# Performance work log

Hardware: AMD Instinct MI355X
Metric: run time of the kernel (lower is better)

The kernel has to match this reference:

```python
import jax, jax.numpy as jnp
import numpy as np

N = 100000   # nodes
E = 1600000  # edges (before self-loops)
F_IN = 128
H = 64
G = 512      # graphs in batch


def _add_self_loops(edge_index, n):
    loop = jnp.arange(n, dtype=edge_index.dtype)
    src = jnp.concatenate([edge_index[0], loop])
    dst = jnp.concatenate([edge_index[1], loop])
    return src, dst


def _gcn_norm(src, dst, n):
    # PyG GCNConv: deg over targets with self-loops, norm = d^-1/2[src]*d^-1/2[dst]
    deg = jax.ops.segment_sum(jnp.ones_like(dst, dtype=jnp.float32), dst, num_segments=n)
    dinv = jnp.where(deg > 0, jax.lax.rsqrt(deg), 0.0)
    return dinv[src] * dinv[dst]


def _gcn_conv(x, src, dst, norm, W, b):
    xw = x @ W                                # [N, H]
    msg = xw[src] * norm[:, None]             # [E+N, H] gather + scale
    out = jax.ops.segment_sum(msg, dst, num_segments=x.shape[0])
    return out + b


def setup_inputs() -> dict:
    key = jax.random.key(0)
    ks = jax.random.split(key, 9)
    x = jax.random.normal(ks[0], (N, F_IN), dtype=jnp.float32)
    edge_index = jax.random.randint(ks[1], (2, E), 0, N, dtype=jnp.int32)
    batch = jnp.sort(jax.random.randint(ks[2], (N,), 0, G, dtype=jnp.int32))
    s1 = 1.0 / np.sqrt(F_IN)
    s2 = 1.0 / np.sqrt(H)
    W1 = jax.random.uniform(ks[3], (F_IN, H), jnp.float32, -s1, s1)
    b1 = jnp.zeros((H,), jnp.float32)
    W2 = jax.random.uniform(ks[4], (H, H), jnp.float32, -s2, s2)
    b2 = jnp.zeros((H,), jnp.float32)
    Wl = jax.random.uniform(ks[5], (H, 1), jnp.float32, -s2, s2)
    bl = jnp.zeros((1,), jnp.float32)
    return {"x": x, "edge_index": edge_index, "batch": batch,
            "W1": W1, "b1": b1, "W2": W2, "b2": b2, "Wl": Wl, "bl": bl}


def reference(x, edge_index, batch, W1, b1, W2, b2, Wl, bl):
    n = x.shape[0]
    src, dst = _add_self_loops(edge_index, n)
    norm = _gcn_norm(src, dst, n)
    h = jax.nn.relu(_gcn_conv(x, src, dst, norm, W1, b1))
    h = jax.nn.relu(_gcn_conv(h, src, dst, norm, W2, b2))
    # global mean pool over graphs
    sums = jax.ops.segment_sum(h, batch, num_segments=G)          # [G, H]
    cnt = jax.ops.segment_sum(jnp.ones((n,), jnp.float32), batch, num_segments=G)
    pooled = sums / jnp.maximum(cnt, 1.0)[:, None]
    return jax.nn.sigmoid(pooled @ Wl + bl)                        # [G, 1]
```

## Files before the change

kernel.cpp:

```cpp
#include <hip/hip_runtime.h>
#include <hip/hip_bf16.h>
#include <cmath>

#define F_IN 128
#define HDIM 64
#define NPB 128
#define NB1 512
#define CAP 2560

typedef __attribute__((ext_vector_type(8))) short bf16x8;
typedef __attribute__((ext_vector_type(4))) float f32x4;
typedef __attribute__((ext_vector_type(2))) float f32x2;

__device__ __forceinline__ float bf2f(unsigned short u) {
    union { unsigned int i; float f; } v; v.i = ((unsigned int)u) << 16; return v.f;
}
__device__ __forceinline__ unsigned short f2bf(float f) {
    __hip_bfloat16 h = __float2bfloat16(f);
    union { __hip_bfloat16 h; unsigned short u; } c; c.h = h; return c.u;
}
__device__ __forceinline__ unsigned char f2fp8(float f) {
    int p = __builtin_amdgcn_cvt_pk_fp8_f32(f, f, 0, false);
    return (unsigned char)(p & 0xff);
}
__device__ __forceinline__ void fp8x8_acc(uint2 v, float* a) {
    f32x2 f;
    f = __builtin_amdgcn_cvt_pk_f32_fp8(v.x, false); a[0] += f.x; a[1] += f.y;
    f = __builtin_amdgcn_cvt_pk_f32_fp8(v.x, true);  a[2] += f.x; a[3] += f.y;
    f = __builtin_amdgcn_cvt_pk_f32_fp8(v.y, false); a[4] += f.x; a[5] += f.y;
    f = __builtin_amdgcn_cvt_pk_f32_fp8(v.y, true);  a[6] += f.x; a[7] += f.y;
}


__launch_bounds__(256)
__global__ void p0_count(const int* __restrict__ dst, int* __restrict__ blk_cnt,
                         int E, int nbuk, int chunk,
                         const float* __restrict__ W1, const float* __restrict__ W2,
                         unsigned short* __restrict__ w1t, unsigned short* __restrict__ w2t) {
    int tid = threadIdx.x;
    if (blockIdx.x >= NB1) {
        int t = (blockIdx.x - NB1) * 256 + tid;
        if (t < F_IN * 64) {
            int c = t & 63, k = t >> 6;
            w1t[c * F_IN + k] = f2bf(W1[t]);
        } else if (t < F_IN * 64 + HDIM * 64) {
            int u = t - F_IN * 64;
            int c = u & 63, k = u >> 6;
            w2t[c * HDIM + k] = f2bf(W2[u]);
        }
        return;
    }
    __shared__ int hist[1024];
    for (int i = tid; i < nbuk; i += 256) hist[i] = 0;
    __syncthreads();
    int lo = blockIdx.x * chunk, hi = min(E, lo + chunk);
    for (int e = lo + tid; e < hi; e += 256)
        atomicAdd(&hist[dst[e] >> 7], 1);
    __syncthreads();
    for (int i = tid; i < nbuk; i += 256)
        blk_cnt[(size_t)i * NB1 + blockIdx.x] = hist[i];
}


__launch_bounds__(256)
__global__ void p_scan_blocks(int* __restrict__ blk_cnt, int* __restrict__ bucket_cnt,
                              int nbuk, const int* __restrict__ batch,
                              int* __restrict__ gstart, int n, int G) {
    int tid = threadIdx.x;
    if (blockIdx.x >= nbuk) {
        int g = (blockIdx.x - nbuk) * 256 + tid;
        if (g > G) return;
        int lo = 0, hi = n;
        while (lo < hi) {
            int mid = (lo + hi) >> 1;
            if (batch[mid] < g) lo = mid + 1; else hi = mid;
        }
        gstart[g] = lo;
        return;
    }
    __shared__ int sd[256];
    int b = blockIdx.x;
    int2* row = (int2*)(blk_cnt + (size_t)b * NB1);
    int2 v = row[tid];
    int s0 = v.x, s1 = s0 + v.y;
    sd[tid] = s1;
    __syncthreads();
    for (int off = 1; off < 256; off <<= 1) {
        int a = (tid >= off) ? sd[tid - off] : 0;
        __syncthreads();
        sd[tid] += a;
        __syncthreads();
    }
    int base = sd[tid] - s1;
    row[tid] = make_int2(base, base + s0);
    if (tid == 255) bucket_cnt[b] = sd[255];
}


__launch_bounds__(256)
__global__ void p1_place(const int* __restrict__ src, const int* __restrict__ dst,
                         const int* __restrict__ blk_cnt, int* __restrict__ pairs,
                         int E, int nbuk, int chunk) {
    __shared__ int cur[1024];
    int tid = threadIdx.x;
    for (int i = tid; i < nbuk; i += 256)
        cur[i] = i * CAP + blk_cnt[(size_t)i * NB1 + blockIdx.x];
    __syncthreads();
    int lo = blockIdx.x * chunk, hi = min(E, lo + chunk);
    for (int e = lo + tid; e < hi; e += 256) {
        int d = dst[e];
        int pos = atomicAdd(&cur[d >> 7], 1);
        pairs[pos] = (src[e] << 7) | (d & 127);
    }
}


__launch_bounds__(256)
__global__ void p2_csr(const int* __restrict__ pairs, const int* __restrict__ bucket_cnt,
                       float* __restrict__ dinv, int* __restrict__ col,
                       int4* __restrict__ slot_hdr, int n) {
    __shared__ int dl[128];
    __shared__ int sc[128];
    __shared__ int cur[128];
    __shared__ int h64[64];
    __shared__ int s64[64];
    int b = blockIdx.x, tid = threadIdx.x;
    int nlo = b << 7;
    int eb = b * CAP;
    int ee = eb + bucket_cnt[b];
    if (tid < 128) dl[tid] = 0;
    if (tid < 64) h64[tid] = 0;
    __syncthreads();
    for (int e = eb + tid; e < ee; e += 256)
        atomicAdd(&dl[pairs[e] & 127], 1);
    __syncthreads();
    int d0 = 0, excl = 0;
    if (tid < 128) { d0 = dl[tid]; sc[tid] = d0; }
    __syncthreads();
    for (int off = 1; off < 128; off <<= 1) {
        int a = (tid >= off && tid < 128) ? sc[tid - off] : 0;
        __syncthreads();
        if (tid < 128) sc[tid] += a;
        __syncthreads();
    }
    if (tid < 128) {
        excl = sc[tid] - d0;
        int node = nlo + tid;
        float dv = rsqrtf((float)(d0 + 1));
        if (node < n) dinv[node] = dv;
        cur[tid] = eb + excl;
        atomicAdd(&h64[min(d0, 63)], 1);
    }
    __syncthreads();
    if (tid == 0) { int run = 0; for (int i = 0; i < 64; ++i) { s64[i] = run; run += h64[i]; } }
    __syncthreads();
    if (tid < 64) h64[tid] = 0;
    __syncthreads();
    if (tid < 128) {
        int node = nlo + tid;
        int bin = min(d0, 63);
        int pos = s64[bin] + atomicAdd(&h64[bin], 1);
        int4 hdr;
        hdr.x = (node < n) ? node : 0x7fffffff;
        hdr.y = eb + excl;
        hdr.z = d0;
        hdr.w = __float_as_int(rsqrtf((float)(d0 + 1)));
        slot_hdr[nlo + pos] = hdr;
    }
    __syncthreads();
    for (int e = eb + tid; e < ee; e += 256) {
        unsigned int v = (unsigned int)pairs[e];
        int pos = atomicAdd(&cur[v & 127], 1);
        col[pos] = (int)(v >> 7);
    }
}


template <int K>
__launch_bounds__(256)
__global__ void matmul_mfma(const float* __restrict__ X, const unsigned short* __restrict__ Wt,
                            const float* __restrict__ dinv, unsigned char* __restrict__ out,
                            int n) {
    constexpr int KS  = K / 32;
    constexpr int LDX = K + 8;
    __shared__ unsigned short Xs[64 * LDX];
    __shared__ unsigned short Ws[64 * LDX];
    int tid = threadIdx.x;
    int rowbase = blockIdx.x * 64;
    for (int i = tid; i < 64 * (K / 8); i += 256) {
        int r = i / (K / 8), ch = i % (K / 8);
        *(bf16x8*)(Ws + r * LDX + ch * 8) = ((const bf16x8*)Wt)[i];
    }
    {
        const float4* X4 = (const float4*)X;
        for (int i = tid; i < 64 * (K / 4); i += 256) {
            int r = i / (K / 4), k4 = i % (K / 4);
            ushort4 u = { 0, 0, 0, 0 };
            int gr = rowbase + r;
            if (gr < n) {
                float4 v = X4[(size_t)gr * (K / 4) + k4];
                u.x = f2bf(v.x); u.y = f2bf(v.y); u.z = f2bf(v.z); u.w = f2bf(v.w);
            }
            *(ushort4*)(Xs + r * LDX + k4 * 4) = u;
        }
    }
    __syncthreads();
    int wave = tid >> 6, lane = tid & 63;
    int q = lane >> 4, nn = lane & 15;
    f32x4 acc[4] = {{0,0,0,0},{0,0,0,0},{0,0,0,0},{0,0,0,0}};
    int mrow = wave * 16 + nn;
#pragma unroll
    for (int s = 0; s < KS; ++s) {
        bf16x8 af = *(const bf16x8*)(Xs + mrow * LDX + s * 32 + q * 8);
#pragma unroll
        for (int c = 0; c < 4; ++c) {
            bf16x8 bf = *(const bf16x8*)(Ws + (c * 16 + nn) * LDX + s * 32 + q * 8);
            acc[c] = __builtin_amdgcn_mfma_f32_16x16x32_bf16(af, bf, acc[c], 0, 0, 0);
        }
    }
#pragma unroll
    for (int r = 0; r < 4; ++r) {
        int row = rowbase + wave * 16 + q * 4 + r;
        if (row >= n) continue;
        float dv = dinv[row];
#pragma unroll
        for (int c = 0; c < 4; ++c)
            out[(size_t)row * HDIM + c * 16 + nn] = f2fp8(acc[c][r] * dv);
    }
}


__launch_bounds__(256)
__global__ void gather1_mm2(const int4* __restrict__ slot_hdr, const int* __restrict__ col,
                            const uint2* __restrict__ xws, const float* __restrict__ bias,
                            const unsigned short* __restrict__ w2t,
                            unsigned char* __restrict__ out8, int nslots, int n) {
    __shared__ unsigned short Hs[32 * 72];
    __shared__ unsigned short Ws[64 * 72];
    __shared__ int   snode[32];
    __shared__ float sdinv[32];

    int tid = threadIdx.x;
    int ls = tid >> 3;
    int L  = tid & 7;
    int slot = blockIdx.x * 32 + ls;

    for (int i = tid; i < 64 * 8; i += 256) {
        int r = i >> 3, ch = i & 7;
        *(bf16x8*)(Ws + r * 72 + ch * 8) = ((const bf16x8*)w2t)[i];
    }

    int node = 0x7fffffff;
    float dv = 0.0f;
    float a[8] = {0, 0, 0, 0, 0, 0, 0, 0};
    if (slot < nslots) {
        int4 hdr = slot_hdr[slot];
        node = hdr.x;
        if (node < n) {
            int s = hdr.y, end = s + hdr.z;
            dv = __int_as_float(hdr.w);
            fp8x8_acc(xws[(size_t)node * 8 + L], a);
            int e = s;
            for (; e + 8 <= end; e += 8) {
                uint2 v0 = xws[(size_t)col[e + 0] * 8 + L];
                uint2 v1 = xws[(size_t)col[e + 1] * 8 + L];
                uint2 v2 = xws[(size_t)col[e + 2] * 8 + L];
                uint2 v3 = xws[(size_t)col[e + 3] * 8 + L];
                uint2 v4 = xws[(size_t)col[e + 4] * 8 + L];
                uint2 v5 = xws[(size_t)col[e + 5] * 8 + L];
                uint2 v6 = xws[(size_t)col[e + 6] * 8 + L];
                uint2 v7 = xws[(size_t)col[e + 7] * 8 + L];
                fp8x8_acc(v0, a); fp8x8_acc(v1, a); fp8x8_acc(v2, a); fp8x8_acc(v3, a);
                fp8x8_acc(v4, a); fp8x8_acc(v5, a); fp8x8_acc(v6, a); fp8x8_acc(v7, a);
            }
            for (; e < end; ++e)
                fp8x8_acc(xws[(size_t)col[e] * 8 + L], a);
        }
    }
    if (L == 0) { snode[ls] = node; sdinv[ls] = dv; }
    {
        int f0 = L * 8;
        bf16x8 o;
        if (node < n) {
#pragma unroll
            for (int j = 0; j < 8; ++j)
                o[j] = (short)f2bf(fmaxf(fmaf(a[j], dv, bias[f0 + j]), 0.0f));
        } else {
            short z[8] = {0,0,0,0,0,0,0,0};
            o = *(bf16x8*)z;
        }
        *(bf16x8*)(Hs + ls * 72 + L * 8) = o;
    }
    __syncthreads();

    int wave = tid >> 6, lane = tid & 63;
    int q = lane >> 4, nn = lane & 15;
    int mt  = wave & 1;
    int nt0 = (wave >> 1) * 2;
    f32x4 acc[2] = {{0,0,0,0},{0,0,0,0}};
#pragma unroll
    for (int s = 0; s < 2; ++s) {
        bf16x8 af = *(const bf16x8*)(Hs + (mt * 16 + nn) * 72 + s * 32 + q * 8);
#pragma unroll
        for (int t = 0; t < 2; ++t) {
            bf16x8 bf = *(const bf16x8*)(Ws + ((nt0 + t) * 16 + nn) * 72 + s * 32 + q * 8);
            acc[t] = __builtin_amdgcn_mfma_f32_16x16x32_bf16(af, bf, acc[t], 0, 0, 0);
        }
    }
#pragma unroll
    for (int r = 0; r < 4; ++r) {
        int lslot = mt * 16 + q * 4 + r;
        int nd = snode[lslot];
        if (nd >= n) continue;
        float dvr = sdinv[lslot];
#pragma unroll
        for (int t = 0; t < 2; ++t)
            out8[(size_t)nd * HDIM + (nt0 + t) * 16 + nn] = f2fp8(acc[t][r] * dvr);
    }
}


__launch_bounds__(256)
__global__ void csr_gather8_fp8(const int4* __restrict__ slot_hdr, const int* __restrict__ col,
                                const uint2* __restrict__ xws, const float* __restrict__ bias,
                                bf16x8* __restrict__ outb, int nslots, int n) {
    int t = blockIdx.x * 256 + threadIdx.x;
    int slot = t >> 3;
    if (slot >= nslots) return;
    int L = t & 7;
    int4 hdr = slot_hdr[slot];
    int node = hdr.x;
    if (node >= n) return;
    int s = hdr.y, end = s + hdr.z;
    float dv = __int_as_float(hdr.w);

    float a[8] = {0, 0, 0, 0, 0, 0, 0, 0};
    fp8x8_acc(xws[(size_t)node * 8 + L], a);
    int e = s;
    for (; e + 8 <= end; e += 8) {
        uint2 v0 = xws[(size_t)col[e + 0] * 8 + L];
        uint2 v1 = xws[(size_t)col[e + 1] * 8 + L];
        uint2 v2 = xws[(size_t)col[e + 2] * 8 + L];
        uint2 v3 = xws[(size_t)col[e + 3] * 8 + L];
        uint2 v4 = xws[(size_t)col[e + 4] * 8 + L];
        uint2 v5 = xws[(size_t)col[e + 5] * 8 + L];
        uint2 v6 = xws[(size_t)col[e + 6] * 8 + L];
        uint2 v7 = xws[(size_t)col[e + 7] * 8 + L];
        fp8x8_acc(v0, a); fp8x8_acc(v1, a); fp8x8_acc(v2, a); fp8x8_acc(v3, a);
        fp8x8_acc(v4, a); fp8x8_acc(v5, a); fp8x8_acc(v6, a); fp8x8_acc(v7, a);
    }
    for (; e < end; ++e)
        fp8x8_acc(xws[(size_t)col[e] * 8 + L], a);

    int f0 = L * 8;
    bf16x8 o;
#pragma unroll
    for (int j = 0; j < 8; ++j)
        o[j] = (short)f2bf(fmaxf(fmaf(a[j], dv, bias[f0 + j]), 0.0f));
    outb[(size_t)node * 8 + L] = o;
}


__launch_bounds__(256)
__global__ void pool_head(const unsigned short* __restrict__ h, const int* __restrict__ gstart,
                          const float* __restrict__ Wl, const float* __restrict__ bl,
                          float* __restrict__ out, int G) {
    int g = blockIdx.x;
    int s = gstart[g], e = gstart[g + 1];
    int f  = threadIdx.x & 63;
    int rg = threadIdx.x >> 6;
    float acc = 0.0f;
    for (int i = s + rg; i < e; i += 4)
        acc += bf2f(h[(size_t)i * HDIM + f]);
    __shared__ float red[4][HDIM];
    red[rg][f] = acc;
    __syncthreads();
    if (rg == 0) {
        float v = (red[0][f] + red[1][f]) + (red[2][f] + red[3][f]);
        float c = fmaxf((float)(e - s), 1.0f);
        v = v * Wl[f] * (1.0f / c);
#pragma unroll
        for (int off = 32; off; off >>= 1) v += __shfl_down(v, off, 64);
        if (f == 0) out[g] = 1.0f / (1.0f + expf(-(v + bl[0])));
    }
}


extern "C" void kernel_launch(void* const* d_in, const int* in_sizes, int n_in,
                              void* d_out, int out_size, void* d_ws, size_t ws_size,
                              hipStream_t stream) {
    const float* x   = (const float*)d_in[0];
    const int* ei    = (const int*)d_in[1];
    const int* batch = (const int*)d_in[2];
    const float* W1  = (const float*)d_in[3];
    const float* b1  = (const float*)d_in[4];
    const float* W2  = (const float*)d_in[5];
    const float* b2  = (const float*)d_in[6];
    const float* Wl  = (const float*)d_in[7];
    const float* bl  = (const float*)d_in[8];
    float* out = (float*)d_out;

    const int n = in_sizes[0] / F_IN;
    const int E = in_sizes[1] / 2;
    const int G = out_size;

    const int* srcp = ei;
    const int* dstp = ei + E;

    int nbuk = (n + NPB - 1) / NPB;
    int nslots = nbuk * NPB;

    char* wsb = (char*)d_ws;
    auto alloc = [&](size_t bytes) { char* p = wsb; wsb += (bytes + 255) & ~(size_t)255; return p; };
    float* dinv       = (float*)alloc((size_t)n * 4);
    int4*  slot_hdr   = (int4*)alloc((size_t)nslots * 16);
    int*   bucket_cnt = (int*)alloc(1024 * 4);
    int*   blk_cnt    = (int*)alloc((size_t)nbuk * NB1 * 4);
    int*   pairs      = (int*)alloc((size_t)nbuk * CAP * 4);
    int*   colx       = (int*)alloc((size_t)nbuk * CAP * 4);
    unsigned short* w1t  = (unsigned short*)alloc((size_t)F_IN * HDIM * 2);
    unsigned short* w2t  = (unsigned short*)alloc((size_t)HDIM * HDIM * 2);
    unsigned char*  xws8 = (unsigned char*)alloc((size_t)n * HDIM);
    unsigned char*  xws8b= (unsigned char*)alloc((size_t)n * HDIM);
    unsigned short* xh2  = (unsigned short*)alloc((size_t)n * HDIM * 2);
    int*   gstart     = (int*)alloc(((size_t)G + 1) * 4);

    const int TB = 256;
    int gMM  = (n + 63) / 64;
    int chunk = (E + NB1 - 1) / NB1;
    int gG8  = (nslots * 8 + TB - 1) / TB;
    int gS   = (nslots + 31) / 32;

    p0_count<<<NB1 + 48, TB, 0, stream>>>(dstp, blk_cnt, E, nbuk, chunk, W1, W2, w1t, w2t);
    p_scan_blocks<<<nbuk + 3, TB, 0, stream>>>(blk_cnt, bucket_cnt, nbuk, batch, gstart, n, G);
    p1_place<<<NB1, TB, 0, stream>>>(srcp, dstp, blk_cnt, pairs, E, nbuk, chunk);
    p2_csr<<<nbuk, TB, 0, stream>>>(pairs, bucket_cnt, dinv, colx, slot_hdr, n);

    matmul_mfma<F_IN><<<gMM, TB, 0, stream>>>(x, w1t, dinv, xws8, n);
    gather1_mm2<<<gS, TB, 0, stream>>>(slot_hdr, colx, (const uint2*)xws8,
                                       b1, w2t, xws8b, nslots, n);
    csr_gather8_fp8<<<gG8, TB, 0, stream>>>(slot_hdr, colx, (const uint2*)xws8b,
                                            b2, (bf16x8*)xh2, nslots, n);
    pool_head<<<G, TB, 0, stream>>>(xh2, gstart, Wl, bl, out, G);
}
```

Measured before the change: 238.8 us.

## Replace count/scan bucketing with atomic bucket offsets and stage pairs in LDS

Merges the per-block histogram, cross-block scan and placement kernels into one placement kernel. Each block now claims its range within each bucket by doing a global atomicAdd on a per-bucket counter, so two launches and the blk_cnt matrix traffic go away. The CSR build caches the bucket's pairs in shared memory so they are read from global memory only once, and the tail of the neighbor gather becomes one masked 8-wide batch instead of a scalar loop. The cost is nondeterministic edge order within a bucket, which changes the float summation order, plus added LDS use in p2_csr that may lower occupancy.

```diff
diff --git a/kernel.cpp b/kernel.cpp
--- a/kernel.cpp
+++ b/kernel.cpp
@@ -30,46 +30,72 @@
     f = __builtin_amdgcn_cvt_pk_f32_fp8(v.y, false); a[4] += f.x; a[5] += f.y;
     f = __builtin_amdgcn_cvt_pk_f32_fp8(v.y, true);  a[6] += f.x; a[7] += f.y;
 }
-
-
-__launch_bounds__(256)
-__global__ void p0_count(const int* __restrict__ dst, int* __restrict__ blk_cnt,
-                         int E, int nbuk, int chunk,
-                         const float* __restrict__ W1, const float* __restrict__ W2,
-                         unsigned short* __restrict__ w1t, unsigned short* __restrict__ w2t) {
-    int tid = threadIdx.x;
-    if (blockIdx.x >= NB1) {
-        int t = (blockIdx.x - NB1) * 256 + tid;
-        if (t < F_IN * 64) {
-            int c = t & 63, k = t >> 6;
-            w1t[c * F_IN + k] = f2bf(W1[t]);
-        } else if (t < F_IN * 64 + HDIM * 64) {
-            int u = t - F_IN * 64;
-            int c = u & 63, k = u >> 6;
-            w2t[c * HDIM + k] = f2bf(W2[u]);
-        }
+__device__ __forceinline__ void fp8x8_acc_m(uint2 v, float m, float* a) {
+    f32x2 f;
+    f = __builtin_amdgcn_cvt_pk_f32_fp8(v.x, false); a[0] = fmaf(f.x, m, a[0]); a[1] = fmaf(f.y, m, a[1]);
+    f = __builtin_amdgcn_cvt_pk_f32_fp8(v.x, true);  a[2] = fmaf(f.x, m, a[2]); a[3] = fmaf(f.y, m, a[3]);
+    f = __builtin_amdgcn_cvt_pk_f32_fp8(v.y, false); a[4] = fmaf(f.x, m, a[4]); a[5] = fmaf(f.y, m, a[5]);
+    f = __builtin_amdgcn_cvt_pk_f32_fp8(v.y, true);  a[6] = fmaf(f.x, m, a[6]); a[7] = fmaf(f.y, m, a[7]);
+}
+
+__device__ __forceinline__ void gather_rows(const int* __restrict__ col,
+                                            const uint2* __restrict__ xws,
+                                            int L, int s, int end, float* a) {
+    int e = s;
+    for (; e + 8 <= end; e += 8) {
+        uint2 v0 = xws[(size_t)col[e + 0] * 8 + L];
+        uint2 v1 = xws[(size_t)col[e + 1] * 8 + L];
+        uint2 v2 = xws[(size_t)col[e + 2] * 8 + L];
+        uint2 v3 = xws[(size_t)col[e + 3] * 8 + L];
+        uint2 v4 = xws[(size_t)col[e + 4] * 8 + L];
+        uint2 v5 = xws[(size_t)col[e + 5] * 8 + L];
+        uint2 v6 = xws[(size_t)col[e + 6] * 8 + L];
+        uint2 v7 = xws[(size_t)col[e + 7] * 8 + L];
+        fp8x8_acc(v0, a); fp8x8_acc(v1, a); fp8x8_acc(v2, a); fp8x8_acc(v3, a);
+        fp8x8_acc(v4, a); fp8x8_acc(v5, a); fp8x8_acc(v6, a); fp8x8_acc(v7, a);
+    }
+    if (e < end) {
+        int last = end - 1;
+        uint2 v0 = xws[(size_t)col[e]               * 8 + L];
+        uint2 v1 = xws[(size_t)col[min(e + 1, last)] * 8 + L];
+        uint2 v2 = xws[(size_t)col[min(e + 2, last)] * 8 + L];
+        uint2 v3 = xws[(size_t)col[min(e + 3, last)] * 8 + L];
+        uint2 v4 = xws[(size_t)col[min(e + 4, last)] * 8 + L];
+        uint2 v5 = xws[(size_t)col[min(e + 5, last)] * 8 + L];
+        uint2 v6 = xws[(size_t)col[min(e + 6, last)] * 8 + L];
+        uint2 v7 = xws[(size_t)col[min(e + 7, last)] * 8 + L];
+        fp8x8_acc(v0, a);
+        fp8x8_acc_m(v1, (e + 1 < end) ? 1.0f : 0.0f, a);
+        fp8x8_acc_m(v2, (e + 2 < end) ? 1.0f : 0.0f, a);
+        fp8x8_acc_m(v3, (e + 3 < end) ? 1.0f : 0.0f, a);
+        fp8x8_acc_m(v4, (e + 4 < end) ? 1.0f : 0.0f, a);
+        fp8x8_acc_m(v5, (e + 5 < end) ? 1.0f : 0.0f, a);
+        fp8x8_acc_m(v6, (e + 6 < end) ? 1.0f : 0.0f, a);
+        fp8x8_acc_m(v7, (e + 7 < end) ? 1.0f : 0.0f, a);
+    }
+}
+
+
+__launch_bounds__(256)
+__global__ void k_init(const float* __restrict__ W1, const float* __restrict__ W2,
+                       unsigned short* __restrict__ w1t, unsigned short* __restrict__ w2t,
+                       const int* __restrict__ batch, int* __restrict__ gstart,
+                       int n, int G, int* __restrict__ gcnt) {
+    int t = blockIdx.x * 256 + threadIdx.x;
+    if (t < F_IN * 64) {
+        int c = t & 63, k = t >> 6;
+        w1t[c * F_IN + k] = f2bf(W1[t]);
         return;
     }
-    __shared__ int hist[1024];
-    for (int i = tid; i < nbuk; i += 256) hist[i] = 0;
-    __syncthreads();
-    int lo = blockIdx.x * chunk, hi = min(E, lo + chunk);
-    for (int e = lo + tid; e < hi; e += 256)
-        atomicAdd(&hist[dst[e] >> 7], 1);
-    __syncthreads();
-    for (int i = tid; i < nbuk; i += 256)
-        blk_cnt[(size_t)i * NB1 + blockIdx.x] = hist[i];
-}
-
-
-__launch_bounds__(256)
-__global__ void p_scan_blocks(int* __restrict__ blk_cnt, int* __restrict__ bucket_cnt,
-                              int nbuk, const int* __restrict__ batch,
-                              int* __restrict__ gstart, int n, int G) {
-    int tid = threadIdx.x;
-    if (blockIdx.x >= nbuk) {
-        int g = (blockIdx.x - nbuk) * 256 + tid;
-        if (g > G) return;
+    t -= F_IN * 64;
+    if (t < HDIM * 64) {
+        int c = t & 63, k = t >> 6;
+        w2t[c * HDIM + k] = f2bf(W2[t]);
+        return;
+    }
+    t -= HDIM * 64;
+    if (t <= G) {
+        int g = t;
         int lo = 0, hi = n;
         while (lo < hi) {
             int mid = (lo + hi) >> 1;
@@ -78,35 +104,29 @@
         gstart[g] = lo;
         return;
     }
-    __shared__ int sd[256];
-    int b = blockIdx.x;
-    int2* row = (int2*)(blk_cnt + (size_t)b * NB1);
-    int2 v = row[tid];
-    int s0 = v.x, s1 = s0 + v.y;
-    sd[tid] = s1;
-    __syncthreads();
-    for (int off = 1; off < 256; off <<= 1) {
-        int a = (tid >= off) ? sd[tid - off] : 0;
-        __syncthreads();
-        sd[tid] += a;
-        __syncthreads();
-    }
-    int base = sd[tid] - s1;
-    row[tid] = make_int2(base, base + s0);
-    if (tid == 255) bucket_cnt[b] = sd[255];
-}
-
-
-__launch_bounds__(256)
-__global__ void p1_place(const int* __restrict__ src, const int* __restrict__ dst,
-                         const int* __restrict__ blk_cnt, int* __restrict__ pairs,
-                         int E, int nbuk, int chunk) {
+    t -= G + 1;
+    if (t < 1024) gcnt[t] = 0;
+}
+
+
+__launch_bounds__(256)
+__global__ void p_place(const int* __restrict__ src, const int* __restrict__ dst,
+                        int* __restrict__ gcnt, int* __restrict__ pairs,
+                        int E, int nbuk, int chunk) {
+    __shared__ int hist[1024];
     __shared__ int cur[1024];
     int tid = threadIdx.x;
-    for (int i = tid; i < nbuk; i += 256)
-        cur[i] = i * CAP + blk_cnt[(size_t)i * NB1 + blockIdx.x];
+    for (int i = tid; i < nbuk; i += 256) hist[i] = 0;
     __syncthreads();
     int lo = blockIdx.x * chunk, hi = min(E, lo + chunk);
+    for (int e = lo + tid; e < hi; e += 256)
+        atomicAdd(&hist[dst[e] >> 7], 1);
+    __syncthreads();
+    for (int i = tid; i < nbuk; i += 256) {
+        int c = hist[i];
+        cur[i] = i * CAP + (c ? atomicAdd(&gcnt[i], c) : 0);
+    }
+    __syncthreads();
     for (int e = lo + tid; e < hi; e += 256) {
         int d = dst[e];
         int pos = atomicAdd(&cur[d >> 7], 1);
@@ -119,6 +139,7 @@
 __global__ void p2_csr(const int* __restrict__ pairs, const int* __restrict__ bucket_cnt,
                        float* __restrict__ dinv, int* __restrict__ col,
                        int4* __restrict__ slot_hdr, int n) {
+    __shared__ int plds[CAP];
     __shared__ int dl[128];
     __shared__ int sc[128];
     __shared__ int cur[128];
@@ -127,12 +148,15 @@
     int b = blockIdx.x, tid = threadIdx.x;
     int nlo = b << 7;
     int eb = b * CAP;
-    int ee = eb + bucket_cnt[b];
+    int cnt = bucket_cnt[b];
     if (tid < 128) dl[tid] = 0;
     if (tid < 64) h64[tid] = 0;
     __syncthreads();
-    for (int e = eb + tid; e < ee; e += 256)
-        atomicAdd(&dl[pairs[e] & 127], 1);
+    for (int i = tid; i < cnt; i += 256) {
+        int v = pairs[eb + i];
+        plds[i] = v;
+        atomicAdd(&dl[v & 127], 1);
+    }
     __syncthreads();
     int d0 = 0, excl = 0;
     if (tid < 128) { d0 = dl[tid]; sc[tid] = d0; }
@@ -146,8 +170,7 @@
     if (tid < 128) {
         excl = sc[tid] - d0;
         int node = nlo + tid;
-        float dv = rsqrtf((float)(d0 + 1));
-        if (node < n) dinv[node] = dv;
+        if (node < n) dinv[node] = rsqrtf((float)(d0 + 1));
         cur[tid] = eb + excl;
         atomicAdd(&h64[min(d0, 63)], 1);
     }
@@ -168,8 +191,8 @@
         slot_hdr[nlo + pos] = hdr;
     }
     __syncthreads();
-    for (int e = eb + tid; e < ee; e += 256) {
-        unsigned int v = (unsigned int)pairs[e];
+    for (int i = tid; i < cnt; i += 256) {
+        unsigned int v = (unsigned int)plds[i];
         int pos = atomicAdd(&cur[v & 127], 1);
         col[pos] = (int)(v >> 7);
     }
@@ -257,24 +280,9 @@
         int4 hdr = slot_hdr[slot];
         node = hdr.x;
         if (node < n) {
-            int s = hdr.y, end = s + hdr.z;
             dv = __int_as_float(hdr.w);
             fp8x8_acc(xws[(size_t)node * 8 + L], a);
-            int e = s;
-            for (; e + 8 <= end; e += 8) {
-                uint2 v0 = xws[(size_t)col[e + 0] * 8 + L];
-                uint2 v1 = xws[(size_t)col[e + 1] * 8 + L];
-                uint2 v2 = xws[(size_t)col[e + 2] * 8 + L];
-                uint2 v3 = xws[(size_t)col[e + 3] * 8 + L];
-                uint2 v4 = xws[(size_t)col[e + 4] * 8 + L];
-                uint2 v5 = xws[(size_t)col[e + 5] * 8 + L];
-                uint2 v6 = xws[(size_t)col[e + 6] * 8 + L];
-                uint2 v7 = xws[(size_t)col[e + 7] * 8 + L];
-                fp8x8_acc(v0, a); fp8x8_acc(v1, a); fp8x8_acc(v2, a); fp8x8_acc(v3, a);
-                fp8x8_acc(v4, a); fp8x8_acc(v5, a); fp8x8_acc(v6, a); fp8x8_acc(v7, a);
-            }
-            for (; e < end; ++e)
-                fp8x8_acc(xws[(size_t)col[e] * 8 + L], a);
+            gather_rows(col, xws, L, hdr.y, hdr.y + hdr.z, a);
         }
     }
     if (L == 0) { snode[ls] = node; sdinv[ls] = dv; }
@@ -331,26 +339,11 @@
     int4 hdr = slot_hdr[slot];
     int node = hdr.x;
     if (node >= n) return;
-    int s = hdr.y, end = s + hdr.z;
     float dv = __int_as_float(hdr.w);
 
     float a[8] = {0, 0, 0, 0, 0, 0, 0, 0};
     fp8x8_acc(xws[(size_t)node * 8 + L], a);
-    int e = s;
-    for (; e + 8 <= end; e += 8) {
-        uint2 v0 = xws[(size_t)col[e + 0] * 8 + L];
-        uint2 v1 = xws[(size_t)col[e + 1] * 8 + L];
-        uint2 v2 = xws[(size_t)col[e + 2] * 8 + L];
-        uint2 v3 = xws[(size_t)col[e + 3] * 8 + L];
-        uint2 v4 = xws[(size_t)col[e + 4] * 8 + L];
-        uint2 v5 = xws[(size_t)col[e + 5] * 8 + L];
-        uint2 v6 = xws[(size_t)col[e + 6] * 8 + L];
-        uint2 v7 = xws[(size_t)col[e + 7] * 8 + L];
-        fp8x8_acc(v0, a); fp8x8_acc(v1, a); fp8x8_acc(v2, a); fp8x8_acc(v3, a);
-        fp8x8_acc(v4, a); fp8x8_acc(v5, a); fp8x8_acc(v6, a); fp8x8_acc(v7, a);
-    }
-    for (; e < end; ++e)
-        fp8x8_acc(xws[(size_t)col[e] * 8 + L], a);
+    gather_rows(col, xws, L, hdr.y, hdr.y + hdr.z, a);
 
     int f0 = L * 8;
     bf16x8 o;
@@ -414,8 +407,7 @@
     auto alloc = [&](size_t bytes) { char* p = wsb; wsb += (bytes + 255) & ~(size_t)255; return p; };
     float* dinv       = (float*)alloc((size_t)n * 4);
     int4*  slot_hdr   = (int4*)alloc((size_t)nslots * 16);
-    int*   bucket_cnt = (int*)alloc(1024 * 4);
-    int*   blk_cnt    = (int*)alloc((size_t)nbuk * NB1 * 4);
+    int*   gcnt       = (int*)alloc(1024 * 4);
     int*   pairs      = (int*)alloc((size_t)nbuk * CAP * 4);
     int*   colx       = (int*)alloc((size_t)nbuk * CAP * 4);
     unsigned short* w1t  = (unsigned short*)alloc((size_t)F_IN * HDIM * 2);
@@ -430,12 +422,12 @@
     int chunk = (E + NB1 - 1) / NB1;
     int gG8  = (nslots * 8 + TB - 1) / TB;
     int gS   = (nslots + 31) / 32;
-
-    p0_count<<<NB1 + 48, TB, 0, stream>>>(dstp, blk_cnt, E, nbuk, chunk, W1, W2, w1t, w2t);
-    p_scan_blocks<<<nbuk + 3, TB, 0, stream>>>(blk_cnt, bucket_cnt, nbuk, batch, gstart, n, G);
-    p1_place<<<NB1, TB, 0, stream>>>(srcp, dstp, blk_cnt, pairs, E, nbuk, chunk);
-    p2_csr<<<nbuk, TB, 0, stream>>>(pairs, bucket_cnt, dinv, colx, slot_hdr, n);
-
+    int initWork = F_IN * 64 + HDIM * 64 + (G + 1) + 1024;
+    int gInit = (initWork + TB - 1) / TB;
+
+    k_init<<<gInit, TB, 0, stream>>>(W1, W2, w1t, w2t, batch, gstart, n, G, gcnt);
+    p_place<<<NB1, TB, 0, stream>>>(srcp, dstp, gcnt, pairs, E, nbuk, chunk);
+    p2_csr<<<nbuk, TB, 0, stream>>>(pairs, gcnt, dinv, colx, slot_hdr, n);
     matmul_mfma<F_IN><<<gMM, TB, 0, stream>>>(x, w1t, dinv, xws8, n);
     gather1_mm2<<<gS, TB, 0, stream>>>(slot_hdr, colx, (const uint2*)xws8,
                                        b1, w2t, xws8b, nslots, n);
```

Result: faster. 233.0 us (-2.4%).
